# Performance work log

Hardware: AMD Instinct MI355X
Metric: run time of the kernel (lower is better)

Reference implementation:

```python
import jax, jax.numpy as jnp
import numpy as np

B, G, D = 256, 64, 20          # batch, genes per term, subsystem output dim
T3, T2, T1, T0 = 2048, 512, 128, 1  # terms per stratum, deepest first
FAN = 4                        # children per internal term (root gets all T1)
EPS = 1e-5                     # BatchNorm1d eps


def setup_inputs() -> dict:
    key = jax.random.key(0)
    ks = jax.random.split(key, 32)
    def genes(k, T):
        # binary gene perturbation states (column 3 of go_gene_strata_state)
        return (jax.random.uniform(k, (B, T, G)) < 0.5).astype(jnp.float32)
    def lin(kw, kb, T, din):
        # nn.init.uniform_(w, -0.001, 0.001) per DCellSubsystem
        W = jax.random.uniform(kw, (T, din, D), minval=-0.001, maxval=0.001)
        b = jax.random.uniform(kb, (T, D), minval=-0.001, maxval=0.001)
        return W, b
    in3, in2, in1, in0 = G, FAN * D + G, FAN * D + G, T1 * D + G
    W3, b3 = lin(ks[0], ks[1], T3, in3)
    W2, b2 = lin(ks[2], ks[3], T2, in2)
    W1, b1 = lin(ks[4], ks[5], T1, in1)
    W0, b0 = lin(ks[6], ks[7], T0, in0)
    ones = lambda T: jnp.ones((T, D), jnp.float32)
    zeros = lambda T: jnp.zeros((T, D), jnp.float32)
    hw0 = jax.random.normal(ks[8], (T0, D, 1)) * 0.1
    hb0 = jnp.zeros((T0, 1), jnp.float32)
    return {
        'genes3': genes(ks[9], T3), 'genes2': genes(ks[10], T2),
        'genes1': genes(ks[11], T1), 'genes0': genes(ks[12], T0),
        'W3': W3, 'b3': b3, 'g3': ones(T3), 'be3': zeros(T3),
        'W2': W2, 'b2': b2, 'g2': ones(T2), 'be2': zeros(T2),
        'W1': W1, 'b1': b1, 'g1': ones(T1), 'be1': zeros(T1),
        'W0': W0, 'b0': b0, 'g0': ones(T0), 'be0': zeros(T0),
        'hw0': hw0, 'hb0': hb0,
    }


def _subsystem(x, W, b, g, be):
    # Linear -> BatchNorm1d (training mode, batch stats over axis 0) -> Tanh
    z = jnp.einsum('bti,tio->bto', x, W) + b          # [B, T, D]
    mu = jnp.mean(z, axis=0)
    var = jnp.var(z, axis=0)                           # biased, as in torch BN
    zn = (z - mu) * jax.lax.rsqrt(var + EPS)
    return jnp.tanh(zn * g + be)


def reference(genes3, genes2, genes1, genes0,
              W3, b3, g3, be3, W2, b2, g2, be2,
              W1, b1, g1, be1, W0, b0, g0, be0, hw0, hb0):
    # stratum 3 (leaves): input is gene states only
    h3 = _subsystem(genes3, W3, b3, g3, be3)           # [B, T3, D]
    # stratum 2: concat FAN contiguous children + own gene states
    x2 = jnp.concatenate([h3.reshape(B, T2, FAN * D), genes2], axis=-1)
    h2 = _subsystem(x2, W2, b2, g2, be2)               # [B, T2, D]
    x1 = jnp.concatenate([h2.reshape(B, T1, FAN * D), genes1], axis=-1)
    h1 = _subsystem(x1, W1, b1, g1, be1)               # [B, T1, D]
    # root: all T1 children + root gene states
    x0 = jnp.concatenate([h1.reshape(B, T0, T1 * D), genes0], axis=-1)
    h0 = _subsystem(x0, W0, b0, g0, be0)               # [B, 1, D]
    pred = jnp.einsum('bto,toc->btc', h0, hw0) + hb0   # root linear head
    return pred.reshape(B, 1)
```

## Files before the change

### kernel.cpp

```cpp
#include <hip/hip_runtime.h>
#include <hip/hip_fp16.h>


#define DEV static __device__ __forceinline__

constexpr int B_  = 256, G_ = 64, D_ = 20;
constexpr int T3_ = 2048, T2_ = 512, T1_ = 128;
constexpr float EPS_ = 1e-5f;

typedef unsigned char u8;
typedef unsigned long long u64;

constexpr size_t OFF_H3B = 0;
constexpr size_t SZ_H3 = (size_t)T3_ * B_ * D_ * 2;
constexpr size_t OFF_H2B = OFF_H3B + SZ_H3;
constexpr size_t SZ_H2 = (size_t)T2_ * B_ * D_ * 2;
constexpr size_t OFF_H1B = OFF_H2B + SZ_H2;
constexpr size_t SZ_H1 = (size_t)T1_ * B_ * D_ * 2;
constexpr size_t OFF_Z0B = OFF_H1B + SZ_H1;

typedef _Float16 half8_t __attribute__((ext_vector_type(8)));
typedef float f32x4 __attribute__((ext_vector_type(4)));

DEV half8_t as_h8(uint4 u) {
    union { uint4 u4; half8_t h; } c; c.u4 = u; return c.h;
}

DEV half8_t bits8_to_h8(uint byte) {
    uint4 r;
    r.x = ((byte & 1u)        | ((byte & 2u)   << 15)) * 0x3C00u;
    r.y = (((byte >> 2) & 1u) | ((byte & 8u)   << 13)) * 0x3C00u;
    r.z = (((byte >> 4) & 1u) | ((byte & 32u)  << 11)) * 0x3C00u;
    r.w = (((byte >> 6) & 1u) | ((byte & 128u) << 9))  * 0x3C00u;
    return as_h8(r);
}

DEV float fast_tanh(float x) {
    float e = __expf(2.0f * x);
    return fmaf(-2.0f, __builtin_amdgcn_rcpf(e + 1.0f), 1.0f);
}

template <int T, int NCHILD>
__global__ __launch_bounds__(256, 4) void k_gemm(const __half* __restrict__ hsrc,
                                                 const float* __restrict__ genes,
                                                 const float* __restrict__ W,
                                                 const float* __restrict__ g,
                                                 const float* __restrict__ be,
                                                 __half* __restrict__ hout) {
    constexpr int K_IN = NCHILD * 20 + 64;
    constexpr int NK = NCHILD + 2;
    constexpr int STRB = NCHILD ? 200 : 72;
    constexpr int LDSH = (32 * STRB > B_ * D_) ? 32 * STRB : B_ * D_;
    __shared__ __align__(16) __half WT[LDSH];
    __shared__ float gv[D_], bev[D_];
    __shared__ float sred[4][16], qred[4][16];
    __shared__ u64 gmask[B_];

    const int t = blockIdx.x, tid = threadIdx.x;
    const int w = tid >> 6, lane = tid & 63;

    {
        const float* gp = genes + ((size_t)(w * 64) * T + t) * G_ + lane;
        u64 my = 0;
#pragma unroll
        for (int r0 = 0; r0 < 64; r0 += 16) {
            float x[16];
#pragma unroll
            for (int r = 0; r < 16; ++r)
                x[r] = gp[(size_t)(r0 + r) * (T * G_)];
#pragma unroll
            for (int r = 0; r < 16; ++r) {
                u64 m = __ballot(x[r] != 0.0f);
                if (lane == r0 + r) my = m;
            }
        }
        gmask[w * 64 + lane] = my;
    }

    if (NCHILD) {
        uint* WTu = (uint*)WT;
        for (int j = tid; j < 32 * STRB / 2; j += 256) WTu[j] = 0;
        __syncthreads();
    }
    if (tid < D_) { gv[tid] = g[t * D_ + tid]; bev[tid] = be[t * D_ + tid]; }
    const float* Wt = W + (size_t)t * (K_IN * D_);
    for (int j = tid; j < K_IN * D_; j += 256) {
        int k_orig = j / D_, o = j - k_orig * D_;
        int k_lds;
        if (NCHILD && k_orig < NCHILD * D_) {
            int c = k_orig / D_;
            k_lds = c * 32 + (k_orig - c * D_);
        } else {
            k_lds = NCHILD * 32 + (k_orig - NCHILD * D_);
        }
        WT[o * STRB + k_lds] = __float2half(Wt[j]);
    }
    __syncthreads();

    const int quad = lane >> 4, l15 = lane & 15;
    const int nt = w >> 1, mhalf = w & 1;
    const int ocol = nt * 16 + l15;
    const int brow_base = mhalf * 128;
    const int shq = quad * 8;

    half8_t Bf[NK];
#pragma unroll
    for (int ks = 0; ks < NK; ++ks)
        Bf[ks] = as_h8(*(const uint4*)(WT + ocol * STRB + ks * 32 + quad * 8));

    f32x4 acc[8];
#pragma unroll
    for (int mt = 0; mt < 8; ++mt) acc[mt] = (f32x4){0.f, 0.f, 0.f, 0.f};

#pragma unroll
    for (int mt = 0; mt < 8; ++mt) {
        const int bA = brow_base + mt * 16 + l15;
        const u64 gm = gmask[bA];
#pragma unroll
        for (int c = 0; c < NCHILD; ++c) {
            const __half* ap = hsrc + ((size_t)(NCHILD * t + c) * B_ + bA) * D_ + quad * 8;
            uint2 u0 = *(const uint2*)(ap);
            uint2 u1 = *(const uint2*)(ap + 4);
            acc[mt] = __builtin_amdgcn_mfma_f32_16x16x32_f16(
                as_h8(make_uint4(u0.x, u0.y, u1.x, u1.y)), Bf[c], acc[mt], 0, 0, 0);
        }
        acc[mt] = __builtin_amdgcn_mfma_f32_16x16x32_f16(
            bits8_to_h8(((uint)gm >> shq) & 0xFFu), Bf[NCHILD], acc[mt], 0, 0, 0);
        acc[mt] = __builtin_amdgcn_mfma_f32_16x16x32_f16(
            bits8_to_h8(((uint)(gm >> 32) >> shq) & 0xFFu), Bf[NCHILD + 1], acc[mt], 0, 0, 0);
    }

    float s = 0.f, q = 0.f;
#pragma unroll
    for (int mt = 0; mt < 8; ++mt)
#pragma unroll
        for (int r = 0; r < 4; ++r) {
            float z = acc[mt][r];
            s += z; q += z * z;
        }
    s += __shfl_xor(s, 16, 64); q += __shfl_xor(q, 16, 64);
    s += __shfl_xor(s, 32, 64); q += __shfl_xor(q, 32, 64);
    if (lane < 16) { sred[w][lane] = s; qred[w][lane] = q; }
    __syncthreads();
    const float S = sred[2 * nt][l15] + sred[2 * nt + 1][l15];
    const float Q = qred[2 * nt][l15] + qred[2 * nt + 1][l15];
    const float mu  = S * (1.0f / B_);
    const float var = fmaxf(Q * (1.0f / B_) - mu * mu, 0.0f);
    const float rstd = rsqrtf(var + EPS_);
    const int oc = ocol < D_ ? ocol : D_ - 1;
    const float A = rstd * gv[oc];
    const float C = bev[oc] - mu * A;

    if (ocol < D_) {
#pragma unroll
        for (int mt = 0; mt < 8; ++mt)
#pragma unroll
            for (int r = 0; r < 4; ++r) {
                float h = fast_tanh(fmaf(A, acc[mt][r], C));
                int b = brow_base + mt * 16 + quad * 4 + r;
                WT[b * D_ + ocol] = __float2half(h);
            }
    }
    __syncthreads();
    const uint4* src4 = (const uint4*)WT;
    uint4* dst4 = (uint4*)(hout + (size_t)t * (B_ * D_));
    for (int j = tid; j < (B_ * D_) / 8; j += 256) dst4[j] = src4[j];
}

__global__ __launch_bounds__(256, 4) void k_stage0a(const __half* __restrict__ h1,
                                                    const float* __restrict__ genes0,
                                                    const float* __restrict__ W0,
                                                    float* __restrict__ z0p) {
    const int b = blockIdx.x >> 2, s = blockIdx.x & 3, tid = threadIdx.x;
    const int kbase = 640 * s;
    float acc[D_] = {};
#pragma unroll
    for (int j = 0; j < 3; ++j) {
        int kl = tid + 256 * j;
        if (kl < 640) {
            int k = kbase + kl;
            int tt = k / D_, o = k - tt * D_;
            float xk = __half2float(h1[((size_t)tt * B_ + b) * D_ + o]);
            const float4* w = (const float4*)(W0 + (size_t)k * D_);
#pragma unroll
            for (int v = 0; v < D_ / 4; ++v) {
                float4 f = w[v];
                acc[4 * v + 0] = fmaf(xk, f.x, acc[4 * v + 0]);
                acc[4 * v + 1] = fmaf(xk, f.y, acc[4 * v + 1]);
                acc[4 * v + 2] = fmaf(xk, f.z, acc[4 * v + 2]);
                acc[4 * v + 3] = fmaf(xk, f.w, acc[4 * v + 3]);
            }
        }
    }
    if (s == 3 && tid < G_) {
        float xk = genes0[(size_t)b * G_ + tid];
        const float4* w = (const float4*)(W0 + (size_t)(T1_ * D_ + tid) * D_);
#pragma unroll
        for (int v = 0; v < D_ / 4; ++v) {
            float4 f = w[v];
            acc[4 * v + 0] = fmaf(xk, f.x, acc[4 * v + 0]);
            acc[4 * v + 1] = fmaf(xk, f.y, acc[4 * v + 1]);
            acc[4 * v + 2] = fmaf(xk, f.z, acc[4 * v + 2]);
            acc[4 * v + 3] = fmaf(xk, f.w, acc[4 * v + 3]);
        }
    }
    __shared__ float sred[4][D_];
    const int lane = tid & 63, wave = tid >> 6;
#pragma unroll
    for (int off = 32; off; off >>= 1)
#pragma unroll
        for (int o = 0; o < D_; ++o) acc[o] += __shfl_xor(acc[o], off, 64);
    if (lane == 0)
#pragma unroll
        for (int o = 0; o < D_; ++o) sred[wave][o] = acc[o];
    __syncthreads();
    if (tid < D_)
        z0p[((size_t)b * 4 + s) * D_ + tid] =
            sred[0][tid] + sred[1][tid] + sred[2][tid] + sred[3][tid];
}

__global__ __launch_bounds__(256) void k_stage0b(const float* __restrict__ z0p,
                                                 const float* __restrict__ g0,
                                                 const float* __restrict__ be0,
                                                 const float* __restrict__ hw0,
                                                 const float* __restrict__ hb0,
                                                 float* __restrict__ out) {
    const int tid = threadIdx.x;
    float acc[D_] = {};
#pragma unroll
    for (int s = 0; s < 4; ++s) {
        const float4* zp = (const float4*)(z0p + ((size_t)tid * 4 + s) * D_);
#pragma unroll
        for (int v = 0; v < D_ / 4; ++v) {
            float4 f = zp[v];
            acc[4 * v + 0] += f.x; acc[4 * v + 1] += f.y;
            acc[4 * v + 2] += f.z; acc[4 * v + 3] += f.w;
        }
    }
    __shared__ float sred[4][D_], qred[4][D_], Avec[D_], Cvec[D_], hwv[D_ + 1];
    const int lane = tid & 63, wave = tid >> 6;
    float s[D_], q[D_];
#pragma unroll
    for (int o = 0; o < D_; ++o) { s[o] = acc[o]; q[o] = acc[o] * acc[o]; }
#pragma unroll
    for (int off = 32; off; off >>= 1) {
#pragma unroll
        for (int o = 0; o < D_; ++o) {
            s[o] += __shfl_xor(s[o], off, 64);
            q[o] += __shfl_xor(q[o], off, 64);
        }
    }
    if (lane == 0) {
#pragma unroll
        for (int o = 0; o < D_; ++o) { sred[wave][o] = s[o]; qred[wave][o] = q[o]; }
    }
    __syncthreads();
    if (tid < D_) {
        float S = sred[0][tid] + sred[1][tid] + sred[2][tid] + sred[3][tid];
        float Q = qred[0][tid] + qred[1][tid] + qred[2][tid] + qred[3][tid];
        float mu  = S * (1.0f / B_);
        float var = fmaxf(Q * (1.0f / B_) - mu * mu, 0.0f);
        float rstd = rsqrtf(var + EPS_);
        float A = rstd * g0[tid];
        Avec[tid] = A;
        Cvec[tid] = be0[tid] - mu * A;
        hwv[tid] = hw0[tid];
    }
    if (tid == 0) hwv[D_] = hb0[0];
    __syncthreads();
    float pred = hwv[D_];
#pragma unroll
    for (int o = 0; o < D_; ++o) {
        float h = fast_tanh(fmaf(acc[o], Avec[o], Cvec[o]));
        pred = fmaf(h, hwv[o], pred);
    }
    out[tid] = pred;
}

extern "C" void kernel_launch(void* const* d_in, const int* in_sizes, int n_in,
                              void* d_out, int out_size, void* d_ws, size_t ws_size,
                              hipStream_t stream) {
    const float* genes3 = (const float*)d_in[0];
    const float* genes2 = (const float*)d_in[1];
    const float* genes1 = (const float*)d_in[2];
    const float* genes0 = (const float*)d_in[3];
    const float* W3  = (const float*)d_in[4];
    const float* g3  = (const float*)d_in[6];
    const float* be3 = (const float*)d_in[7];
    const float* W2  = (const float*)d_in[8];
    const float* g2  = (const float*)d_in[10];
    const float* be2 = (const float*)d_in[11];
    const float* W1  = (const float*)d_in[12];
    const float* g1  = (const float*)d_in[14];
    const float* be1 = (const float*)d_in[15];
    const float* W0  = (const float*)d_in[16];
    const float* g0  = (const float*)d_in[18];
    const float* be0 = (const float*)d_in[19];
    const float* hw0 = (const float*)d_in[20];
    const float* hb0 = (const float*)d_in[21];

    char* wsb = (char*)d_ws;
    __half* h3  = (__half*)(wsb + OFF_H3B);
    __half* h2  = (__half*)(wsb + OFF_H2B);
    __half* h1  = (__half*)(wsb + OFF_H1B);
    float*  z0p = (float*)(wsb + OFF_Z0B);

    k_gemm<T3_, 0><<<T3_, 256, 0, stream>>>(nullptr, genes3, W3, g3, be3, h3);
    k_gemm<T2_, 4><<<T2_, 256, 0, stream>>>(h3, genes2, W2, g2, be2, h2);
    k_gemm<T1_, 4><<<T1_, 256, 0, stream>>>(h2, genes1, W1, g1, be1, h1);
    k_stage0a<<<B_ * 4, 256, 0, stream>>>(h1, genes0, W0, z0p);
    k_stage0b<<<1, 256, 0, stream>>>(z0p, g0, be0, hw0, hb0, (float*)d_out);
}
```

Measured before the change: 326.2 us.

## Fuse leaf stratum into stratum-2 kernel, keeping child activations in LDS

Replaces the separate stratum-3 and stratum-2 kernels with one kernel per stratum-2 term. Each block computes its four child leaf subsystems (GEMM, BatchNorm, tanh) into shared memory and then runs the stratum-2 GEMM from there. This removes the h3 global write and read round-trip and one launch, and double-buffers the W3 weight staging across children. In exchange there are only 512 blocks, larger LDS use and launch bounds lowered to 2 waves per SIMD, which reduces parallelism.

```diff
diff --git a/kernel.cpp b/kernel.cpp
--- a/kernel.cpp
+++ b/kernel.cpp
@@ -11,9 +11,7 @@
 typedef unsigned char u8;
 typedef unsigned long long u64;
 
-constexpr size_t OFF_H3B = 0;
-constexpr size_t SZ_H3 = (size_t)T3_ * B_ * D_ * 2;
-constexpr size_t OFF_H2B = OFF_H3B + SZ_H3;
+constexpr size_t OFF_H2B = 0;
 constexpr size_t SZ_H2 = (size_t)T2_ * B_ * D_ * 2;
 constexpr size_t OFF_H1B = OFF_H2B + SZ_H2;
 constexpr size_t SZ_H1 = (size_t)T1_ * B_ * D_ * 2;
@@ -38,6 +36,218 @@
 DEV float fast_tanh(float x) {
     float e = __expf(2.0f * x);
     return fmaf(-2.0f, __builtin_amdgcn_rcpf(e + 1.0f), 1.0f);
+}
+
+__global__ __launch_bounds__(256, 2) void k_gemm32(
+        const float* __restrict__ genes3, const float* __restrict__ genes2,
+        const float* __restrict__ W3, const float* __restrict__ g3,
+        const float* __restrict__ be3,
+        const float* __restrict__ W2, const float* __restrict__ g2,
+        const float* __restrict__ be2, __half* __restrict__ h2out) {
+    constexpr int STRB3 = 72, STRB2 = 200;
+    __shared__ __align__(16) __half h3loc[4 * B_ * D_ + 16];
+    __shared__ __align__(16) __half WT3[2][32 * STRB3];
+    __shared__ __align__(16) __half WT2[32 * STRB2];
+    __shared__ u64 gmask[5][B_];
+    __shared__ float sredb[2][4][16], qredb[2][4][16];
+    __shared__ float gv3[4 * D_], bev3[4 * D_], gv2[D_], bev2[D_];
+
+    const int t = blockIdx.x, tid = threadIdx.x;
+    const int w = tid >> 6, lane = tid & 63;
+
+    const int rb = w * 64;
+#pragma unroll
+    for (int s = 0; s < 5; ++s) {
+        const float* gp = (s < 4)
+            ? genes3 + ((size_t)rb * T3_ + 4 * t + s) * G_ + lane
+            : genes2 + ((size_t)rb * T2_ + t) * G_ + lane;
+        const size_t str = (size_t)(s < 4 ? T3_ : T2_) * G_;
+        u64 my = 0;
+#pragma unroll
+        for (int r0 = 0; r0 < 64; r0 += 16) {
+            float x[16];
+#pragma unroll
+            for (int r = 0; r < 16; ++r) x[r] = gp[(size_t)(r0 + r) * str];
+#pragma unroll
+            for (int r = 0; r < 16; ++r) {
+                u64 m = __ballot(x[r] != 0.0f);
+                if (lane == r0 + r) my = m;
+            }
+        }
+        gmask[s][rb + lane] = my;
+    }
+
+    {
+        uint* WTu = (uint*)WT2;
+        for (int j = tid; j < 32 * STRB2 / 2; j += 256) WTu[j] = 0;
+        if (tid < 16) h3loc[4 * B_ * D_ + tid] = __half(0.0f);
+    }
+    __syncthreads();
+
+    if (tid < 4 * D_) {
+        gv3[tid] = g3[(size_t)(4 * t) * D_ + tid];
+        bev3[tid] = be3[(size_t)(4 * t) * D_ + tid];
+    } else if (tid < 5 * D_) {
+        gv2[tid - 4 * D_] = g2[(size_t)t * D_ + (tid - 4 * D_)];
+        bev2[tid - 4 * D_] = be2[(size_t)t * D_ + (tid - 4 * D_)];
+    }
+    {
+        const float* Wt = W2 + (size_t)t * (144 * D_);
+        for (int j = tid; j < 144 * D_; j += 256) {
+            int k_orig = j / D_, o = j - k_orig * D_;
+            int k_lds;
+            if (k_orig < 4 * D_) {
+                int c = k_orig / D_;
+                k_lds = c * 32 + (k_orig - c * D_);
+            } else {
+                k_lds = 4 * 32 + (k_orig - 4 * D_);
+            }
+            WT2[o * STRB2 + k_lds] = __float2half(Wt[j]);
+        }
+        const float* W3t = W3 + (size_t)(4 * t) * (G_ * D_);
+#pragma unroll
+        for (int i = 0; i < 5; ++i) {
+            int j = tid + i * 256;
+            int k = j / D_, o = j - k * D_;
+            WT3[0][o * STRB3 + k] = __float2half(W3t[j]);
+        }
+    }
+    __syncthreads();
+
+    const int quad = lane >> 4, l15 = lane & 15;
+    const int nt = w >> 1, mhalf = w & 1;
+    const int ocol = nt * 16 + l15;
+    const int brow_base = mhalf * 128;
+    const int shq = quad * 8;
+    const int oc = ocol < D_ ? ocol : D_ - 1;
+
+#pragma unroll
+    for (int c = 0; c < 4; ++c) {
+        float wreg[5];
+        if (c < 3) {
+            const float* W3n = W3 + (size_t)(4 * t + c + 1) * (G_ * D_);
+#pragma unroll
+            for (int i = 0; i < 5; ++i) wreg[i] = W3n[tid + i * 256];
+        }
+        const __half* WTc = WT3[c & 1];
+        half8_t Bf0 = as_h8(*(const uint4*)(WTc + ocol * STRB3 + quad * 8));
+        half8_t Bf1 = as_h8(*(const uint4*)(WTc + ocol * STRB3 + 32 + quad * 8));
+
+        f32x4 acc[8];
+#pragma unroll
+        for (int mt = 0; mt < 8; ++mt) acc[mt] = (f32x4){0.f, 0.f, 0.f, 0.f};
+#pragma unroll
+        for (int mt = 0; mt < 8; ++mt) {
+            const int bA = brow_base + mt * 16 + l15;
+            const u64 gm = gmask[c][bA];
+            acc[mt] = __builtin_amdgcn_mfma_f32_16x16x32_f16(
+                bits8_to_h8(((uint)gm >> shq) & 0xFFu), Bf0, acc[mt], 0, 0, 0);
+            acc[mt] = __builtin_amdgcn_mfma_f32_16x16x32_f16(
+                bits8_to_h8(((uint)(gm >> 32) >> shq) & 0xFFu), Bf1, acc[mt], 0, 0, 0);
+        }
+
+        if (c < 3) {
+#pragma unroll
+            for (int i = 0; i < 5; ++i) {
+                int j = tid + i * 256;
+                int k = j / D_, o = j - k * D_;
+                WT3[(c + 1) & 1][o * STRB3 + k] = __float2half(wreg[i]);
+            }
+        }
+
+        float s = 0.f, q = 0.f;
+#pragma unroll
+        for (int mt = 0; mt < 8; ++mt)
+#pragma unroll
+            for (int r = 0; r < 4; ++r) {
+                float z = acc[mt][r];
+                s += z; q += z * z;
+            }
+        s += __shfl_xor(s, 16, 64); q += __shfl_xor(q, 16, 64);
+        s += __shfl_xor(s, 32, 64); q += __shfl_xor(q, 32, 64);
+        if (lane < 16) { sredb[c & 1][w][lane] = s; qredb[c & 1][w][lane] = q; }
+        __syncthreads();
+        const float S = sredb[c & 1][2 * nt][l15] + sredb[c & 1][2 * nt + 1][l15];
+        const float Q = qredb[c & 1][2 * nt][l15] + qredb[c & 1][2 * nt + 1][l15];
+        const float mu  = S * (1.0f / B_);
+        const float var = fmaxf(Q * (1.0f / B_) - mu * mu, 0.0f);
+        const float rstd = rsqrtf(var + EPS_);
+        const float A = rstd * gv3[c * D_ + oc];
+        const float C = bev3[c * D_ + oc] - mu * A;
+        if (ocol < D_) {
+#pragma unroll
+            for (int mt = 0; mt < 8; ++mt)
+#pragma unroll
+                for (int r = 0; r < 4; ++r) {
+                    float h = fast_tanh(fmaf(A, acc[mt][r], C));
+                    int b = brow_base + mt * 16 + quad * 4 + r;
+                    h3loc[(size_t)(c * B_ + b) * D_ + ocol] = __float2half(h);
+                }
+        }
+    }
+    __syncthreads();
+
+    half8_t Bf[6];
+#pragma unroll
+    for (int ks = 0; ks < 6; ++ks)
+        Bf[ks] = as_h8(*(const uint4*)(WT2 + ocol * STRB2 + ks * 32 + quad * 8));
+
+    f32x4 acc[8];
+#pragma unroll
+    for (int mt = 0; mt < 8; ++mt) acc[mt] = (f32x4){0.f, 0.f, 0.f, 0.f};
+#pragma unroll
+    for (int mt = 0; mt < 8; ++mt) {
+        const int bA = brow_base + mt * 16 + l15;
+        const u64 gm = gmask[4][bA];
+#pragma unroll
+        for (int c = 0; c < 4; ++c) {
+            const __half* ap = h3loc + (size_t)(c * B_ + bA) * D_ + quad * 8;
+            uint2 u0 = *(const uint2*)(ap);
+            uint2 u1 = *(const uint2*)(ap + 4);
+            acc[mt] = __builtin_amdgcn_mfma_f32_16x16x32_f16(
+                as_h8(make_uint4(u0.x, u0.y, u1.x, u1.y)), Bf[c], acc[mt], 0, 0, 0);
+        }
+        acc[mt] = __builtin_amdgcn_mfma_f32_16x16x32_f16(
+            bits8_to_h8(((uint)gm >> shq) & 0xFFu), Bf[4], acc[mt], 0, 0, 0);
+        acc[mt] = __builtin_amdgcn_mfma_f32_16x16x32_f16(
+            bits8_to_h8(((uint)(gm >> 32) >> shq) & 0xFFu), Bf[5], acc[mt], 0, 0, 0);
+    }
+
+    float s = 0.f, q = 0.f;
+#pragma unroll
+    for (int mt = 0; mt < 8; ++mt)
+#pragma unroll
+        for (int r = 0; r < 4; ++r) {
+            float z = acc[mt][r];
+            s += z; q += z * z;
+        }
+    s += __shfl_xor(s, 16, 64); q += __shfl_xor(q, 16, 64);
+    s += __shfl_xor(s, 32, 64); q += __shfl_xor(q, 32, 64);
+    if (lane < 16) { sredb[0][w][lane] = s; qredb[0][w][lane] = q; }
+    __syncthreads();
+    const float S = sredb[0][2 * nt][l15] + sredb[0][2 * nt + 1][l15];
+    const float Q = qredb[0][2 * nt][l15] + qredb[0][2 * nt + 1][l15];
+    const float mu  = S * (1.0f / B_);
+    const float var = fmaxf(Q * (1.0f / B_) - mu * mu, 0.0f);
+    const float rstd = rsqrtf(var + EPS_);
+    const float A = rstd * gv2[oc];
+    const float C = bev2[oc] - mu * A;
+
+    __half* ebuf = WT2;
+    if (ocol < D_) {
+#pragma unroll
+        for (int mt = 0; mt < 8; ++mt)
+#pragma unroll
+            for (int r = 0; r < 4; ++r) {
+                float h = fast_tanh(fmaf(A, acc[mt][r], C));
+                int b = brow_base + mt * 16 + quad * 4 + r;
+                ebuf[b * D_ + ocol] = __float2half(h);
+            }
+    }
+    __syncthreads();
+    const uint4* src4 = (const uint4*)ebuf;
+    uint4* dst4 = (uint4*)(h2out + (size_t)t * (B_ * D_));
+    for (int j = tid; j < (B_ * D_) / 8; j += 256) dst4[j] = src4[j];
 }
 
 template <int T, int NCHILD>
@@ -300,13 +510,12 @@
     const float* hb0 = (const float*)d_in[21];
 
     char* wsb = (char*)d_ws;
-    __half* h3  = (__half*)(wsb + OFF_H3B);
     __half* h2  = (__half*)(wsb + OFF_H2B);
     __half* h1  = (__half*)(wsb + OFF_H1B);
     float*  z0p = (float*)(wsb + OFF_Z0B);
 
-    k_gemm<T3_, 0><<<T3_, 256, 0, stream>>>(nullptr, genes3, W3, g3, be3, h3);
-    k_gemm<T2_, 4><<<T2_, 256, 0, stream>>>(h3, genes2, W2, g2, be2, h2);
+    k_gemm32<<<T2_, 256, 0, stream>>>(genes3, genes2, W3, g3, be3,
+                                      W2, g2, be2, h2);
     k_gemm<T1_, 4><<<T1_, 256, 0, stream>>>(h2, genes1, W1, g1, be1, h1);
     k_stage0a<<<B_ * 4, 256, 0, stream>>>(h1, genes0, W0, z0p);
     k_stage0b<<<1, 256, 0, stream>>>(z0p, g0, be0, hw0, hb0, (float*)d_out);
```

After: 318.7 us. 1.02x faster.
